# Performance work log

Measured on AMD Instinct MI355X. Metric: run time of the kernel, lower is better.

## Reference

```python
import jax, jax.numpy as jnp
import numpy as np

NUM_SAMPLED_ROIS = 512
FG_FRACTION = 0.25
FG_IOU_THR = 0.5
BG_IOU_HIGH = 0.5
BG_IOU_LOW = 0.0
IMG_SIZE = 1024.0


def _make_boxes(key, shape):
    kc, ks = jax.random.split(key)
    c = jax.random.uniform(kc, shape + (2,)) * IMG_SIZE            # centers (y, x)
    s = jax.random.uniform(ks, shape + (2,)) * 128.0 + 8.0         # sizes
    lo = jnp.clip(c - s * 0.5, 0.0, IMG_SIZE)
    hi = jnp.clip(c + s * 0.5, 0.0, IMG_SIZE)
    return jnp.concatenate([lo, hi], axis=-1)                       # [ymin, xmin, ymax, xmax]


def setup_inputs() -> dict:
    key = jax.random.key(0)
    k1, k2, k3, k4 = jax.random.split(key, 4)
    B, N, M = 32, 8192, 256
    boxes = _make_boxes(k1, (B, N))
    gt_raw = _make_boxes(k2, (B, M))
    num_valid = jax.random.randint(k3, (B,), 8, M + 1)
    valid = jnp.arange(M)[None, :] < num_valid[:, None]            # [B, M]
    gt_boxes = jnp.where(valid[..., None], gt_raw, -jnp.ones_like(gt_raw))
    cls = jax.random.randint(k4, (B, M), 1, 91, dtype=jnp.int32)
    gt_classes = jnp.where(valid, cls, -jnp.ones_like(cls))
    return {"boxes": boxes, "gt_boxes": gt_boxes, "gt_classes": gt_classes}


def _bbox_overlap(boxes, gt_boxes):
    # boxes [B,N,4], gt_boxes [B,M,4] -> IoU [B,N,M]; invalid (padded) gt -> -1
    b = boxes[:, :, None, :]
    g = gt_boxes[:, None, :, :]
    iy0 = jnp.maximum(b[..., 0], g[..., 0])
    ix0 = jnp.maximum(b[..., 1], g[..., 1])
    iy1 = jnp.minimum(b[..., 2], g[..., 2])
    ix1 = jnp.minimum(b[..., 3], g[..., 3])
    inter = jnp.maximum(iy1 - iy0, 0.0) * jnp.maximum(ix1 - ix0, 0.0)
    area_b = (boxes[..., 2] - boxes[..., 0]) * (boxes[..., 3] - boxes[..., 1])
    area_g = (gt_boxes[..., 2] - gt_boxes[..., 0]) * (gt_boxes[..., 3] - gt_boxes[..., 1])
    union = area_b[:, :, None] + area_g[:, None, :] - inter
    iou = jnp.where(union > 0.0, inter / union, 0.0)
    gt_invalid = jnp.max(gt_boxes, axis=-1) < 0.0                  # [B, M]
    return jnp.where(gt_invalid[:, None, :], -1.0, iou)


def _rank_desc(score):
    # rank of each element when sorted by descending score, per row
    order = jnp.argsort(-score, axis=1)
    return jnp.argsort(order, axis=1)


def _sample_indices(key, positive, negative, num_samples, fg_fraction):
    # balanced fg/bg sampling: up to num_fg random positives, fill rest with negatives
    B, Np = positive.shape
    num_fg = int(num_samples * fg_fraction)
    r = jax.random.uniform(key, (B, Np))
    pos_rank = _rank_desc(jnp.where(positive, r, -1.0))
    sel_pos = positive & (pos_rank < num_fg)
    n_pos = jnp.sum(sel_pos, axis=1, keepdims=True)
    neg_rank = _rank_desc(jnp.where(negative, r, -1.0))
    sel_neg = negative & (neg_rank < (num_samples - n_pos))
    selected = sel_pos | sel_neg
    # prefer selected candidates; random tie-break fills any shortfall
    score = selected.astype(jnp.float32) * 2.0 + r
    _, idx = jax.lax.top_k(score, num_samples)
    return idx                                                      # [B, K]


def reference(boxes, gt_boxes, gt_classes):
    gt_boxes = gt_boxes.astype(boxes.dtype)
    boxes = jnp.concatenate([boxes, gt_boxes], axis=1)              # mix gt boxes
    iou = _bbox_overlap(boxes, gt_boxes)                            # [B, N', M]

    matched_vals = jnp.max(iou, axis=-1)                            # [B, N']
    matched_idx = jnp.argmax(iou, axis=-1).astype(jnp.int32)
    indicator = jnp.where(
        matched_vals >= FG_IOU_THR, 1,
        jnp.where(matched_vals >= BG_IOU_HIGH, -2,
                  jnp.where(matched_vals >= BG_IOU_LOW, -1, -3)))

    positive = indicator >= 0
    negative = indicator == -1
    ignored = indicator == -2
    invalid = indicator == -3
    background = negative | invalid                                 # [B, N']

    g_cls = jnp.take_along_axis(gt_classes, matched_idx, axis=1)
    matched_gt_classes = jnp.where(background, 0, g_cls)
    g_box = jnp.take_along_axis(gt_boxes, matched_idx[..., None], axis=1)
    matched_gt_boxes = jnp.where(background[..., None], 0.0, g_box)
    matched_gt_indices = jnp.where(background, -1, matched_idx)

    idx = _sample_indices(jax.random.key(42), positive, negative & ~ignored,
                          NUM_SAMPLED_ROIS, FG_FRACTION)

    sampled_rois = jnp.take_along_axis(boxes, idx[..., None], axis=1)
    sampled_gt_boxes = jnp.take_along_axis(matched_gt_boxes, idx[..., None], axis=1)
    sampled_gt_classes = jnp.take_along_axis(matched_gt_classes, idx, axis=1)
    sampled_gt_indices = jnp.take_along_axis(matched_gt_indices, idx, axis=1)
    return sampled_rois, sampled_gt_boxes, sampled_gt_classes, sampled_gt_indices
```

## Files before the change

kernel.cpp:

```cpp
#include <hip/hip_runtime.h>
#include <stdint.h>

#define BATCH 32
#define NBOX 8192
#define MGT 256
#define NP 8448
#define NUM_SAMP 512
#define NUM_FG 128
#define NBUCK 2048
#define CANDCAP 1024

__device__ __forceinline__ uint32_t rotl32(uint32_t x, uint32_t r) {
  return (x << r) | (x >> (32u - r));
}

__device__ __forceinline__ uint32_t threefry_bits(uint32_t f) {
  uint32_t x0 = 0u;
  uint32_t x1 = f;
  const uint32_t ks0 = 0u, ks1 = 42u;
  const uint32_t ks2 = 0x1BD11BDAu ^ ks0 ^ ks1;
  const uint32_t k[3] = {ks0, ks1, ks2};
  x0 += ks0; x1 += ks1;
  const uint32_t rotA[4] = {13u, 15u, 26u, 6u};
  const uint32_t rotB[4] = {17u, 29u, 16u, 24u};
#pragma unroll
  for (int g = 0; g < 5; ++g) {
#pragma unroll
    for (int q = 0; q < 4; ++q) {
      uint32_t rr = (g & 1) ? rotB[q] : rotA[q];
      x0 += x1; x1 = rotl32(x1, rr); x1 ^= x0;
    }
    x0 += k[(g + 1) % 3];
    x1 += k[(g + 2) % 3] + (uint32_t)(g + 1);
  }
  return x0 ^ x1;
}

__global__ __launch_bounds__(256) void k1_compute(const float* __restrict__ boxes,
                                                  const float* __restrict__ gt_boxes,
                                                  uint32_t* __restrict__ packed,
                                                  int* __restrict__ midx_ws) {
  const int b = blockIdx.y;
  const int i = blockIdx.x * 256 + threadIdx.x;

  __shared__ int nv_s;
  if (threadIdx.x == 0) nv_s = MGT;
  __syncthreads();
  {
    const int j = threadIdx.x;
    float g0 = gt_boxes[(b * MGT + j) * 4];
    if (g0 < 0.0f) atomicMin(&nv_s, j);
  }
  __syncthreads();
  const int nv = nv_s;

  float4 bx;
  if (i < NBOX) bx = ((const float4*)boxes)[b * NBOX + i];
  else          bx = ((const float4*)gt_boxes)[b * MGT + (i - NBOX)];
  const float area_b = __fmul_rn(__fsub_rn(bx.z, bx.x), __fsub_rn(bx.w, bx.y));

  const double CHALF = 0.5 - 0x1p-26;
  float bestq = -1.0f;
  int bestj = -1;
  const float4* grow = (const float4*)(gt_boxes + (size_t)b * MGT * 4);
#pragma unroll 4
  for (int j = 0; j < nv; ++j) {
    float4 g = grow[j];
    float iy0 = fmaxf(bx.x, g.x);
    float ix0 = fmaxf(bx.y, g.y);
    float iy1 = fminf(bx.z, g.z);
    float ix1 = fminf(bx.w, g.w);
    float ih = fmaxf(__fsub_rn(iy1, iy0), 0.0f);
    float iw = fmaxf(__fsub_rn(ix1, ix0), 0.0f);
    float inter = __fmul_rn(ih, iw);
    if (inter > 0.0f) {
      float ag = __fmul_rn(__fsub_rn(g.z, g.x), __fsub_rn(g.w, g.y));
      float u = __fsub_rn(__fadd_rn(area_b, ag), inter);
      if ((double)inter >= (double)u * CHALF) {
        float q = __fdiv_rn(inter, u);
        if (q > bestq) { bestq = q; bestj = j; }
      }
    }
  }

  const bool pos = (bestj >= 0);
  const uint32_t bits = threefry_bits((uint32_t)(b * NP + i));
  const uint32_t mant = bits >> 9;
  const uint32_t inv = 0x7FFFFFu - mant;
  packed[b * NP + i] = (inv << 1) | (pos ? 1u : 0u);
  midx_ws[b * NP + i] = bestj;
}

__device__ __forceinline__ void emit_lds(unsigned long long* __restrict__ sk,
                                         int* __restrict__ cnt,
                                         uint32_t idx, uint32_t inv) {
  uint32_t mant = 0x7FFFFFu - inv;
  float r = __uint_as_float(0x3F800000u | mant) - 1.0f;
  float score = __fadd_rn(2.0f, r);
  uint32_t sb = __float_as_uint(score);
  unsigned long long key =
      ((unsigned long long)(~sb) << 14) | (unsigned long long)idx;
  int slot = atomicAdd(cnt, 1);
  if (slot < NUM_SAMP) sk[slot] = key;
}

__global__ __launch_bounds__(256) void k23_select_sort_gather(
    const uint32_t* __restrict__ packed, const float* __restrict__ boxes,
    const float* __restrict__ gt_boxes, const int* __restrict__ gt_classes,
    const int* __restrict__ midx_ws, float* __restrict__ out) {
  const int b = blockIdx.x;
  const int tid = threadIdx.x;
  __shared__ uint32_t srow[NP];
  __shared__ uint32_t hist[2][NBUCK];
  __shared__ uint32_t part[256];
  __shared__ unsigned long long cand[2][CANDCAP];
  __shared__ unsigned long long sk[NUM_SAMP];
  __shared__ int candn[2];
  __shared__ int cutb[2], rem[2];
  __shared__ int npos_s, selcnt_s;

  if (tid == 0) { selcnt_s = 0; candn[0] = 0; candn[1] = 0; }
  {
    const uint4* row4 = (const uint4*)(packed + b * NP);
    for (int k = tid; k < NP / 4; k += 256) ((uint4*)srow)[k] = row4[k];
    uint32_t* hf = &hist[0][0];
    for (int k = tid; k < 2 * NBUCK; k += 256) hf[k] = 0;
  }
  __syncthreads();

  for (int idx = tid; idx < NP; idx += 256) {
    uint32_t w = srow[idx];
    atomicAdd(&hist[w & 1u][(w >> 1) >> 12], 1u);
  }
  __syncthreads();

  for (int fpass = 0; fpass < 2; ++fpass) {
    const int f = 1 - fpass;
    uint32_t csum = 0;
#pragma unroll
    for (int q = 0; q < 8; ++q) csum += hist[f][tid * 8 + q];
    part[tid] = csum;
    __syncthreads();
    for (int off = 1; off < 256; off <<= 1) {
      uint32_t v = part[tid];
      uint32_t add = (tid >= off) ? part[tid - off] : 0u;
      __syncthreads();
      part[tid] = v + add;
      __syncthreads();
    }
    const uint32_t incl = part[tid];
    const uint32_t excl = incl - csum;
    if (f == 1 && tid == 255) npos_s = (int)incl;
    __syncthreads();
    const int npos_c = (npos_s < NUM_FG) ? npos_s : NUM_FG;
    const uint32_t L = (f == 1) ? (uint32_t)NUM_FG
                                : (uint32_t)(NUM_SAMP - npos_c);
    if (excl < L && incl >= L) {
      uint32_t run = excl;
#pragma unroll
      for (int q = 0; q < 8; ++q) {
        uint32_t h = hist[f][tid * 8 + q];
        if (run + h >= L) { cutb[f] = tid * 8 + q; rem[f] = (int)(L - run); break; }
        run += h;
      }
    }
    if (tid == 255 && incl < L) {
      cutb[f] = NBUCK; rem[f] = 0;
    }
    __syncthreads();
  }

  for (int idx = tid; idx < NP; idx += 256) {
    uint32_t w = srow[idx];
    uint32_t f = w & 1u;
    uint32_t inv = w >> 1;
    int bk = (int)(inv >> 12);
    if (bk < cutb[f]) {
      emit_lds(sk, &selcnt_s, (uint32_t)idx, inv);
    } else if (bk == cutb[f]) {
      int s = atomicAdd(&candn[f], 1);
      if (s < CANDCAP)
        cand[f][s] = ((unsigned long long)inv << 14) | (unsigned long long)idx;
    }
  }
  __syncthreads();

  for (int f = 0; f < 2; ++f) {
    int n = candn[f]; if (n > CANDCAP) n = CANDCAP;
    for (int c = tid; c < n; c += 256) {
      unsigned long long me = cand[f][c];
      int r = 0;
      for (int j = 0; j < n; ++j) r += (cand[f][j] < me) ? 1 : 0;
      if (r < rem[f])
        emit_lds(sk, &selcnt_s, (uint32_t)(me & 0x3FFFull),
                 (uint32_t)(me >> 14));
    }
  }
  __syncthreads();

  for (int k = 2; k <= NUM_SAMP; k <<= 1) {
    for (int j = k >> 1; j > 0; j >>= 1) {
      for (int t = tid; t < NUM_SAMP; t += 256) {
        int ixj = t ^ j;
        if (ixj > t) {
          unsigned long long a = sk[t], c = sk[ixj];
          bool asc = ((t & k) == 0);
          if ((a > c) == asc) { sk[t] = c; sk[ixj] = a; }
        }
      }
      __syncthreads();
    }
  }

  const int gtb_base = BATCH * NUM_SAMP * 4;
  const int cls_base = 2 * BATCH * NUM_SAMP * 4;
  const int idx_base = cls_base + BATCH * NUM_SAMP;

  for (int t = tid; t < NUM_SAMP; t += 256) {
    unsigned long long key = sk[t];
    int i = (int)(key & 0x3FFFull);
    if (i >= NP) i = NP - 1;
    float4 roi;
    if (i < NBOX) roi = ((const float4*)boxes)[b * NBOX + i];
    else          roi = ((const float4*)gt_boxes)[b * MGT + (i - NBOX)];
    const int o4 = (b * NUM_SAMP + t) * 4;
    out[o4 + 0] = roi.x;
    out[o4 + 1] = roi.y;
    out[o4 + 2] = roi.z;
    out[o4 + 3] = roi.w;

    const int midx = midx_ws[b * NP + i];
    float4 gb = make_float4(0.0f, 0.0f, 0.0f, 0.0f);
    float cls = 0.0f;
    if (midx >= 0) {
      gb = ((const float4*)gt_boxes)[b * MGT + midx];
      cls = (float)gt_classes[b * MGT + midx];
    }
    out[gtb_base + o4 + 0] = gb.x;
    out[gtb_base + o4 + 1] = gb.y;
    out[gtb_base + o4 + 2] = gb.z;
    out[gtb_base + o4 + 3] = gb.w;
    out[cls_base + b * NUM_SAMP + t] = cls;
    out[idx_base + b * NUM_SAMP + t] = (float)midx;
  }
}

extern "C" void kernel_launch(void* const* d_in, const int* in_sizes, int n_in,
                              void* d_out, int out_size, void* d_ws, size_t ws_size,
                              hipStream_t stream) {
  const float* boxes      = (const float*)d_in[0];
  const float* gt_boxes   = (const float*)d_in[1];
  const int*   gt_classes = (const int*)d_in[2];
  float* out = (float*)d_out;

  char* ws = (char*)d_ws;
  uint32_t* packed = (uint32_t*)(ws);
  int* midx_ws     = (int*)(ws + 1081344);

  k1_compute<<<dim3(NP / 256, BATCH), 256, 0, stream>>>(boxes, gt_boxes, packed,
                                                        midx_ws);
  k23_select_sort_gather<<<BATCH, 256, 0, stream>>>(packed, boxes, gt_boxes,
                                                    gt_classes, midx_ws, out);
}
```

Baseline: 121.9 us.

## Stage GT boxes in LDS, merge histograms, wave-scan, 512-thread select kernel

The IoU kernel now stages the batch's GT boxes and their areas in shared memory, so the inner loop reads LDS instead of global memory and no longer recomputes GT areas. The select kernel runs with 512 threads and packs the positive and negative histograms into one 32-bit counter array (high and low 16 bits). A single wave-shuffle prefix scan replaces the two barrier-heavy block scans. The bitonic sort uses one element per thread and only a wave barrier for intra-wave strides, cutting block-wide syncs; sk is pre-filled with sentinels so unfilled slots sort last.

Result: faster. 106.6 us (-12.6%).

```diff
diff --git a/kernel.cpp b/kernel.cpp
--- a/kernel.cpp
+++ b/kernel.cpp
@@ -42,14 +42,17 @@
                                                   int* __restrict__ midx_ws) {
   const int b = blockIdx.y;
   const int i = blockIdx.x * 256 + threadIdx.x;
-
+  __shared__ float4 sg[MGT];
+  __shared__ float sga[MGT];
   __shared__ int nv_s;
   if (threadIdx.x == 0) nv_s = MGT;
   __syncthreads();
   {
     const int j = threadIdx.x;
-    float g0 = gt_boxes[(b * MGT + j) * 4];
-    if (g0 < 0.0f) atomicMin(&nv_s, j);
+    float4 g = ((const float4*)gt_boxes)[b * MGT + j];
+    sg[j] = g;
+    sga[j] = __fmul_rn(__fsub_rn(g.z, g.x), __fsub_rn(g.w, g.y));
+    if (g.x < 0.0f) atomicMin(&nv_s, j);
   }
   __syncthreads();
   const int nv = nv_s;
@@ -62,10 +65,9 @@
   const double CHALF = 0.5 - 0x1p-26;
   float bestq = -1.0f;
   int bestj = -1;
-  const float4* grow = (const float4*)(gt_boxes + (size_t)b * MGT * 4);
 #pragma unroll 4
   for (int j = 0; j < nv; ++j) {
-    float4 g = grow[j];
+    float4 g = sg[j];
     float iy0 = fmaxf(bx.x, g.x);
     float ix0 = fmaxf(bx.y, g.y);
     float iy1 = fminf(bx.z, g.z);
@@ -74,8 +76,7 @@
     float iw = fmaxf(__fsub_rn(ix1, ix0), 0.0f);
     float inter = __fmul_rn(ih, iw);
     if (inter > 0.0f) {
-      float ag = __fmul_rn(__fsub_rn(g.z, g.x), __fsub_rn(g.w, g.y));
-      float u = __fsub_rn(__fadd_rn(area_b, ag), inter);
+      float u = __fsub_rn(__fadd_rn(area_b, sga[j]), inter);
       if ((double)inter >= (double)u * CHALF) {
         float q = __fdiv_rn(inter, u);
         if (q > bestq) { bestq = q; bestj = j; }
@@ -104,15 +105,15 @@
   if (slot < NUM_SAMP) sk[slot] = key;
 }
 
-__global__ __launch_bounds__(256) void k23_select_sort_gather(
+__global__ __launch_bounds__(512) void k23_select_sort_gather(
     const uint32_t* __restrict__ packed, const float* __restrict__ boxes,
     const float* __restrict__ gt_boxes, const int* __restrict__ gt_classes,
     const int* __restrict__ midx_ws, float* __restrict__ out) {
   const int b = blockIdx.x;
   const int tid = threadIdx.x;
   __shared__ uint32_t srow[NP];
-  __shared__ uint32_t hist[2][NBUCK];
-  __shared__ uint32_t part[256];
+  __shared__ uint32_t hist[NBUCK];
+  __shared__ uint32_t wsum[8];
   __shared__ unsigned long long cand[2][CANDCAP];
   __shared__ unsigned long long sk[NUM_SAMP];
   __shared__ int candn[2];
@@ -122,55 +123,79 @@
   if (tid == 0) { selcnt_s = 0; candn[0] = 0; candn[1] = 0; }
   {
     const uint4* row4 = (const uint4*)(packed + b * NP);
-    for (int k = tid; k < NP / 4; k += 256) ((uint4*)srow)[k] = row4[k];
-    uint32_t* hf = &hist[0][0];
-    for (int k = tid; k < 2 * NBUCK; k += 256) hf[k] = 0;
-  }
-  __syncthreads();
-
-  for (int idx = tid; idx < NP; idx += 256) {
+    for (int k = tid; k < NP / 4; k += 512) ((uint4*)srow)[k] = row4[k];
+    for (int k = tid; k < NBUCK; k += 512) hist[k] = 0;
+    if (tid < NUM_SAMP) sk[tid] = ~0ull;
+  }
+  __syncthreads();
+
+  for (int idx = tid; idx < NP; idx += 512) {
     uint32_t w = srow[idx];
-    atomicAdd(&hist[w & 1u][(w >> 1) >> 12], 1u);
-  }
-  __syncthreads();
-
-  for (int fpass = 0; fpass < 2; ++fpass) {
-    const int f = 1 - fpass;
-    uint32_t csum = 0;
-#pragma unroll
-    for (int q = 0; q < 8; ++q) csum += hist[f][tid * 8 + q];
-    part[tid] = csum;
-    __syncthreads();
-    for (int off = 1; off < 256; off <<= 1) {
-      uint32_t v = part[tid];
-      uint32_t add = (tid >= off) ? part[tid - off] : 0u;
-      __syncthreads();
-      part[tid] = v + add;
-      __syncthreads();
-    }
-    const uint32_t incl = part[tid];
-    const uint32_t excl = incl - csum;
-    if (f == 1 && tid == 255) npos_s = (int)incl;
-    __syncthreads();
-    const int npos_c = (npos_s < NUM_FG) ? npos_s : NUM_FG;
-    const uint32_t L = (f == 1) ? (uint32_t)NUM_FG
-                                : (uint32_t)(NUM_SAMP - npos_c);
-    if (excl < L && incl >= L) {
-      uint32_t run = excl;
-#pragma unroll
-      for (int q = 0; q < 8; ++q) {
-        uint32_t h = hist[f][tid * 8 + q];
-        if (run + h >= L) { cutb[f] = tid * 8 + q; rem[f] = (int)(L - run); break; }
+    atomicAdd(&hist[(w >> 1) >> 12], (w & 1u) ? 0x10000u : 1u);
+  }
+  __syncthreads();
+
+  const int base = tid * 4;
+  uint32_t csum = 0;
+#pragma unroll
+  for (int q = 0; q < 4; ++q) csum += hist[base + q];
+  uint32_t incl = csum;
+#pragma unroll
+  for (int d = 1; d < 64; d <<= 1) {
+    uint32_t v = __shfl_up(incl, d, 64);
+    if ((tid & 63) >= d) incl += v;
+  }
+  const int wid = tid >> 6;
+  if ((tid & 63) == 63) wsum[wid] = incl;
+  __syncthreads();
+  {
+    uint32_t prefix = 0;
+#pragma unroll
+    for (int w = 0; w < 8; ++w) prefix += (w < wid) ? wsum[w] : 0u;
+    incl += prefix;
+  }
+  const uint32_t excl = incl - csum;
+  if (tid == 511) {
+    const int tpos = (int)(incl >> 16);
+    const int tneg = (int)(incl & 0xFFFFu);
+    npos_s = tpos;
+    if (tpos < NUM_FG) { cutb[1] = NBUCK; rem[1] = 0; }
+    const int npc = (tpos < NUM_FG) ? tpos : NUM_FG;
+    const int Ln = NUM_SAMP - npc;
+    if (Ln == 0)        { cutb[0] = -1;    rem[0] = 0; }
+    else if (tneg < Ln) { cutb[0] = NBUCK; rem[0] = 0; }
+  }
+  __syncthreads();
+  {
+    const uint32_t L = NUM_FG;
+    uint32_t pe = excl >> 16, pi = incl >> 16;
+    if (pe < L && pi >= L) {
+      uint32_t run = pe;
+#pragma unroll
+      for (int q = 0; q < 4; ++q) {
+        uint32_t h = hist[base + q] >> 16;
+        if (run + h >= L) { cutb[1] = base + q; rem[1] = (int)(L - run); break; }
         run += h;
       }
     }
-    if (tid == 255 && incl < L) {
-      cutb[f] = NBUCK; rem[f] = 0;
-    }
-    __syncthreads();
-  }
-
-  for (int idx = tid; idx < NP; idx += 256) {
+  }
+  {
+    const int npc = (npos_s < NUM_FG) ? npos_s : NUM_FG;
+    const uint32_t L = (uint32_t)(NUM_SAMP - npc);
+    uint32_t ne = excl & 0xFFFFu, ni = incl & 0xFFFFu;
+    if (L > 0 && ne < L && ni >= L) {
+      uint32_t run = ne;
+#pragma unroll
+      for (int q = 0; q < 4; ++q) {
+        uint32_t h = hist[base + q] & 0xFFFFu;
+        if (run + h >= L) { cutb[0] = base + q; rem[0] = (int)(L - run); break; }
+        run += h;
+      }
+    }
+  }
+  __syncthreads();
+
+  for (int idx = tid; idx < NP; idx += 512) {
     uint32_t w = srow[idx];
     uint32_t f = w & 1u;
     uint32_t inv = w >> 1;
@@ -187,7 +212,7 @@
 
   for (int f = 0; f < 2; ++f) {
     int n = candn[f]; if (n > CANDCAP) n = CANDCAP;
-    for (int c = tid; c < n; c += 256) {
+    for (int c = tid; c < n; c += 512) {
       unsigned long long me = cand[f][c];
       int r = 0;
       for (int j = 0; j < n; ++j) r += (cand[f][j] < me) ? 1 : 0;
@@ -196,27 +221,29 @@
                  (uint32_t)(me >> 14));
     }
   }
-  __syncthreads();
-
+
+  bool prevCross = true;
   for (int k = 2; k <= NUM_SAMP; k <<= 1) {
     for (int j = k >> 1; j > 0; j >>= 1) {
-      for (int t = tid; t < NUM_SAMP; t += 256) {
-        int ixj = t ^ j;
-        if (ixj > t) {
-          unsigned long long a = sk[t], c = sk[ixj];
-          bool asc = ((t & k) == 0);
-          if ((a > c) == asc) { sk[t] = c; sk[ixj] = a; }
-        }
-      }
-      __syncthreads();
-    }
-  }
+      const bool cross = (j >= 64);
+      if (cross || prevCross) __syncthreads();
+      else __builtin_amdgcn_wave_barrier();
+      const int t = tid, ixj = t ^ j;
+      if (ixj > t) {
+        unsigned long long a = sk[t], c = sk[ixj];
+        bool asc = ((t & k) == 0);
+        if ((a > c) == asc) { sk[t] = c; sk[ixj] = a; }
+      }
+      prevCross = cross;
+    }
+  }
+  __syncthreads();
 
   const int gtb_base = BATCH * NUM_SAMP * 4;
   const int cls_base = 2 * BATCH * NUM_SAMP * 4;
   const int idx_base = cls_base + BATCH * NUM_SAMP;
 
-  for (int t = tid; t < NUM_SAMP; t += 256) {
+  for (int t = tid; t < NUM_SAMP; t += 512) {
     unsigned long long key = sk[t];
     int i = (int)(key & 0x3FFFull);
     if (i >= NP) i = NP - 1;
@@ -259,6 +286,6 @@
 
   k1_compute<<<dim3(NP / 256, BATCH), 256, 0, stream>>>(boxes, gt_boxes, packed,
                                                         midx_ws);
-  k23_select_sort_gather<<<BATCH, 256, 0, stream>>>(packed, boxes, gt_boxes,
+  k23_select_sort_gather<<<BATCH, 512, 0, stream>>>(packed, boxes, gt_boxes,
                                                     gt_classes, midx_ws, out);
 }
```
